# Optimization experiments

Hardware: AMD Instinct MI355X
Metric: run time of the kernel (lower is better)

The kernel has to match this reference:

```python
import jax, jax.numpy as jnp
import numpy as np

D_MODEL = 1024
NUM_HEADS = 16
HEAD_DIM = D_MODEL // NUM_HEADS
B, S = 2, 2048


def setup_inputs() -> dict:
    key = jax.random.key(0)
    ks = jax.random.split(key, 16)
    sd = 1.0 / np.sqrt(D_MODEL)
    def lin(k):
        kw, kb = jax.random.split(k)
        W = jax.random.uniform(kw, (D_MODEL, D_MODEL), jnp.float32, -sd, sd)
        b = jax.random.uniform(kb, (D_MODEL,), jnp.float32, -sd, sd)
        return W, b
    Wq, bq = lin(ks[0]); Wk, bk = lin(ks[1]); Wv, bv = lin(ks[2]); Wo, bo = lin(ks[3])
    return {
        'q': jax.random.normal(ks[4], (B, S, D_MODEL), jnp.float32),
        'k': jax.random.normal(ks[5], (B, S, D_MODEL), jnp.float32),
        'v': jax.random.normal(ks[6], (B, S, D_MODEL), jnp.float32),
        'phase': jax.random.normal(ks[7], (B,), jnp.float32),
        'Wq': Wq, 'bq': bq, 'Wk': Wk, 'bk': bk, 'Wv': Wv, 'bv': bv, 'Wo': Wo, 'bo': bo,
        'phase_coupling': jnp.zeros((1, NUM_HEADS, 1, 1), jnp.float32),
        'attention_scale': jnp.ones((1,), jnp.float32),
        'stability_factor': jnp.ones((1,), jnp.float32),
    }


def reference(q, k, v, phase, Wq, bq, Wk, bk, Wv, bv, Wo, bo,
              phase_coupling, attention_scale, stability_factor):
    batch, seq, _ = q.shape
    scale = HEAD_DIM ** -0.5

    def split_heads(x):  # [B,S,D] -> [B,H,S,hd]
        return x.reshape(batch, -1, NUM_HEADS, HEAD_DIM).transpose(0, 2, 1, 3)

    qh = split_heads(q @ Wq.T + bq)
    kh = split_heads(k @ Wk.T + bk)
    vh = split_heads(v @ Wv.T + bv)

    scores = jnp.einsum('bhqd,bhkd->bhqk', qh, kh) * (scale * attention_scale)
    # phase modulation: phase [B] -> [B,1,1,1]; scores *= 1 + coupling*sin(phase)
    phase_factor = jnp.sin(phase)[:, None, None, None]
    scores = scores * (1.0 + phase_coupling * phase_factor)

    attn_weights = jax.nn.softmax(scores, axis=-1)  # dropout is identity in eval
    out = jnp.einsum('bhqk,bhkd->bhqd', attn_weights, vh)
    out = out.transpose(0, 2, 1, 3).reshape(batch, seq, D_MODEL)
    out = (out @ Wo.T + bo) * stability_factor
    return out, attn_weights
```

## Files before the change

kernel.cpp:

```cpp
#include <hip/hip_runtime.h>
#include <hip/hip_bf16.h>
#include <cstdint>
#include <cstddef>

#define NH 16
#define HD 64
#define SS 2048
#define DM 1024
#define MTOT 4096

typedef __attribute__((ext_vector_type(8))) short short8;
typedef __attribute__((ext_vector_type(4))) float float4v;
typedef __attribute__((ext_vector_type(4))) int int4v;
typedef __attribute__((ext_vector_type(4))) unsigned short ushort4v;

__device__ __forceinline__ unsigned short f2bf(float f){
  unsigned int u = __builtin_bit_cast(unsigned int, f);
  u += 0x7FFFu + ((u >> 16) & 1u);
  return (unsigned short)(u >> 16);
}

__device__ __forceinline__ void gload16(const void* g, void* l){
  __builtin_amdgcn_global_load_lds((const __attribute__((address_space(1))) void*)g,
                                   (__attribute__((address_space(3))) void*)l, 16, 0, 0);
}

__global__ __launch_bounds__(256) void cvt_kernel(const float* __restrict__ src,
                                                  unsigned short* __restrict__ dst, int n){
  for (int i = (blockIdx.x*blockDim.x + threadIdx.x)*4; i < n; i += gridDim.x*blockDim.x*4){
    float4v v = *reinterpret_cast<const float4v*>(src + i);
    ushort4v o;
    o.x = f2bf(v.x); o.y = f2bf(v.y); o.z = f2bf(v.z); o.w = f2bf(v.w);
    *reinterpret_cast<ushort4v*>(dst + i) = o;
  }
}

template<int MODE>
__global__ __launch_bounds__(256) void gemm_bt(const unsigned short* __restrict__ A,
                                               const unsigned short* __restrict__ Bw,
                                               const float* __restrict__ bias,
                                               void* __restrict__ outp,
                                               int M, int N, int K,
                                               const float* __restrict__ oscale_p){
  __shared__ unsigned short Alds[128*32];
  __shared__ unsigned short Blds[128*32];
  const int t = threadIdx.x;
  const int l = t & 63;
  const int w = t >> 6;
  const int m0 = blockIdx.y * 128, n0 = blockIdx.x * 128;
  const int wm = (w & 1)*64, wn = (w >> 1)*64;
  const int srow = t >> 2;
  const int scol = (t & 3)*8;
  const int lr = l & 15, lg = l >> 4;
  float4v acc[4][4] = {};
  for (int k0 = 0; k0 < K; k0 += 32){
    __syncthreads();
    gload16(A  + (size_t)(m0 + srow     )*K + k0 + scol, Alds + t*8);
    gload16(A  + (size_t)(m0 + srow + 64)*K + k0 + scol, Alds + 2048 + t*8);
    gload16(Bw + (size_t)(n0 + srow     )*K + k0 + scol, Blds + t*8);
    gload16(Bw + (size_t)(n0 + srow + 64)*K + k0 + scol, Blds + 2048 + t*8);
    asm volatile("s_waitcnt vmcnt(0)" ::: "memory");
    __syncthreads();
    short8 afrag[4], bfrag[4];
    #pragma unroll
    for (int mb = 0; mb < 4; ++mb)
      afrag[mb] = *reinterpret_cast<const short8*>(Alds + (wm + mb*16 + lr)*32 + lg*8);
    #pragma unroll
    for (int nb = 0; nb < 4; ++nb)
      bfrag[nb] = *reinterpret_cast<const short8*>(Blds + (wn + nb*16 + lr)*32 + lg*8);
    #pragma unroll
    for (int mb = 0; mb < 4; ++mb)
      #pragma unroll
      for (int nb = 0; nb < 4; ++nb)
        acc[mb][nb] = __builtin_amdgcn_mfma_f32_16x16x32_bf16(afrag[mb], bfrag[nb], acc[mb][nb], 0, 0, 0);
  }
  const float osc = (MODE == 2) ? oscale_p[0] : 1.0f;
  #pragma unroll
  for (int mb = 0; mb < 4; ++mb){
    #pragma unroll
    for (int nb = 0; nb < 4; ++nb){
      const int gn = n0 + wn + nb*16 + lr;
      const float biasv = bias[gn];
      #pragma unroll
      for (int r = 0; r < 4; ++r){
        const int gm = m0 + wm + mb*16 + lg*4 + r;
        float v = acc[mb][nb][r] + biasv;
        if (MODE == 2){
          reinterpret_cast<float*>(outp)[(size_t)gm*N + gn] = v * osc;
        } else {
          const int b_ = gm >> 11, s_ = gm & 2047, h_ = gn >> 6, d_ = gn & 63;
          unsigned short* o = reinterpret_cast<unsigned short*>(outp);
          if (MODE == 0)
            o[((size_t)(b_*NH + h_)*SS + s_)*HD + d_] = f2bf(v);
          else
            o[((size_t)(b_*NH + h_)*HD + d_)*SS + s_] = f2bf(v);
        }
      }
    }
  }
}

__global__ __launch_bounds__(256, 4) void attn_kernel(
    const unsigned short* __restrict__ Qh,
    const unsigned short* __restrict__ Kh,
    const unsigned short* __restrict__ Vt,
    unsigned short* __restrict__ AO,
    float* __restrict__ attnW,
    const float* __restrict__ phase,
    const float* __restrict__ pc,
    const float* __restrict__ ascale)
{
  __shared__ float mred[4][32], lred[4][32];
  __shared__ __attribute__((aligned(16))) float ored[4][32*32];

  const int t = threadIdx.x;
  const int w = t >> 6, l = t & 63;
  const int lr = l & 15, lg = l >> 4;
  const int bh = blockIdx.x, qt = blockIdx.y;
  const int b = bh >> 4, h = bh & 15;
  const int q0 = qt*32;
  const float scale_eff = 0.125f * ascale[0] * (1.0f + pc[h] * sinf(phase[b]));

  const unsigned short* qbase = Qh + ((size_t)bh*SS + q0 + lr)*HD + lg*8;
  short8 aq[2][2];
  aq[0][0] = *reinterpret_cast<const short8*>(qbase);
  aq[0][1] = *reinterpret_cast<const short8*>(qbase + 32);
  aq[1][0] = *reinterpret_cast<const short8*>(qbase + 16*HD);
  aq[1][1] = *reinterpret_cast<const short8*>(qbase + 16*HD + 32);

  const int tbase = w * 512;
  const unsigned short* kbase = Kh + ((size_t)bh*SS + tbase + lr)*HD + lg*8;

  float m[2] = {-1e30f, -1e30f}, lsum[2] = {0.f, 0.f};
  #pragma unroll 2
  for (int tb = 0; tb < 32; ++tb){
    const unsigned short* kp = kbase + (size_t)tb*16*HD;
    short8 bk0 = *reinterpret_cast<const short8*>(kp);
    short8 bk1 = *reinterpret_cast<const short8*>(kp + 32);
    #pragma unroll
    for (int qs = 0; qs < 2; ++qs){
      float4v pacc = {};
      pacc = __builtin_amdgcn_mfma_f32_16x16x32_bf16(bk0, aq[qs][0], pacc, 0, 0, 0);
      pacc = __builtin_amdgcn_mfma_f32_16x16x32_bf16(bk1, aq[qs][1], pacc, 0, 0, 0);
      const float s0 = pacc[0]*scale_eff, s1 = pacc[1]*scale_eff;
      const float s2 = pacc[2]*scale_eff, s3 = pacc[3]*scale_eff;
      const float smax = fmaxf(fmaxf(s0, s1), fmaxf(s2, s3));
      const float nm = fmaxf(m[qs], smax);
      lsum[qs] = lsum[qs]*__expf(m[qs] - nm)
               + __expf(s0 - nm) + __expf(s1 - nm) + __expf(s2 - nm) + __expf(s3 - nm);
      m[qs] = nm;
    }
  }
  #pragma unroll
  for (int mask = 16; mask < 64; mask <<= 1){
    #pragma unroll
    for (int qs = 0; qs < 2; ++qs){
      float om = __shfl_xor(m[qs], mask, 64);
      float ol = __shfl_xor(lsum[qs], mask, 64);
      float nm = fmaxf(m[qs], om);
      lsum[qs] = lsum[qs]*__expf(m[qs] - nm) + ol*__expf(om - nm);
      m[qs] = nm;
    }
  }
  if (l < 16){
    mred[w][lr] = m[0];      lred[w][lr] = lsum[0];
    mred[w][16+lr] = m[1];   lred[w][16+lr] = lsum[1];
  }
  __syncthreads();
  float rm[2], rrl[2];
  #pragma unroll
  for (int qs = 0; qs < 2; ++qs){
    const int row = qs*16 + lr;
    float fm = mred[0][row], fl = lred[0][row];
    #pragma unroll
    for (int ww = 1; ww < 4; ++ww){
      float om = mred[ww][row], ol = lred[ww][row];
      float nm = fmaxf(fm, om);
      fl = fl*__expf(fm - nm) + ol*__expf(om - nm);
      fm = nm;
    }
    rm[qs] = fm; rrl[qs] = 1.0f/fl;
  }

  float4v oacc[2][4] = {};
  float* gwq0 = attnW + ((size_t)bh*SS + q0 + lr)*SS + tbase;
  float* gwq1 = gwq0 + (size_t)16*SS;
  const unsigned short* vbase = Vt + ((size_t)bh*HD + lr)*SS + tbase + lg*8;
  const int idxA = (((lg & 1)*2)*16 + lr)*4;
  const int idxB = idxA + 64;
  const bool hi = (lg >= 2);

  for (int tp = 0; tp < 16; ++tp){
    const int tloc = tp*32;
    const unsigned short* kpA = kbase + (size_t)tloc*HD;
    short8 k0A = *reinterpret_cast<const short8*>(kpA);
    short8 k1A = *reinterpret_cast<const short8*>(kpA + 32);
    short8 k0B = *reinterpret_cast<const short8*>(kpA + 16*HD);
    short8 k1B = *reinterpret_cast<const short8*>(kpA + 16*HD + 32);
    short8 bv[4];
    #pragma unroll
    for (int dt = 0; dt < 4; ++dt)
      bv[dt] = *reinterpret_cast<const short8*>(vbase + (size_t)(dt*16)*SS + tloc);

    #pragma unroll
    for (int qs = 0; qs < 2; ++qs){
      float4v pA = {};
      pA = __builtin_amdgcn_mfma_f32_16x16x32_bf16(k0A, aq[qs][0], pA, 0, 0, 0);
      pA = __builtin_amdgcn_mfma_f32_16x16x32_bf16(k1A, aq[qs][1], pA, 0, 0, 0);
      float4v pB = {};
      pB = __builtin_amdgcn_mfma_f32_16x16x32_bf16(k0B, aq[qs][0], pB, 0, 0, 0);
      pB = __builtin_amdgcn_mfma_f32_16x16x32_bf16(k1B, aq[qs][1], pB, 0, 0, 0);
      float4v eA, eB;
      eA.x = __expf(pA[0]*scale_eff - rm[qs])*rrl[qs];
      eA.y = __expf(pA[1]*scale_eff - rm[qs])*rrl[qs];
      eA.z = __expf(pA[2]*scale_eff - rm[qs])*rrl[qs];
      eA.w = __expf(pA[3]*scale_eff - rm[qs])*rrl[qs];
      eB.x = __expf(pB[0]*scale_eff - rm[qs])*rrl[qs];
      eB.y = __expf(pB[1]*scale_eff - rm[qs])*rrl[qs];
      eB.z = __expf(pB[2]*scale_eff - rm[qs])*rrl[qs];
      eB.w = __expf(pB[3]*scale_eff - rm[qs])*rrl[qs];
      const int w0A = ((int)f2bf(eA.y) << 16) | (int)f2bf(eA.x);
      const int w1A = ((int)f2bf(eA.w) << 16) | (int)f2bf(eA.z);
      const int w0B = ((int)f2bf(eB.y) << 16) | (int)f2bf(eB.x);
      const int w1B = ((int)f2bf(eB.w) << 16) | (int)f2bf(eB.z);

      const int a0 = __builtin_amdgcn_ds_bpermute(idxA, w0A);
      const int b0 = __builtin_amdgcn_ds_bpermute(idxA, w0B);
      const int a1 = __builtin_amdgcn_ds_bpermute(idxA, w1A);
      const int b1 = __builtin_amdgcn_ds_bpermute(idxA, w1B);
      const int a2 = __builtin_amdgcn_ds_bpermute(idxB, w0A);
      const int b2 = __builtin_amdgcn_ds_bpermute(idxB, w0B);
      const int a3 = __builtin_amdgcn_ds_bpermute(idxB, w1A);
      const int b3 = __builtin_amdgcn_ds_bpermute(idxB, w1B);
      int4v words;
      words.x = hi ? b0 : a0;
      words.y = hi ? b1 : a1;
      words.z = hi ? b2 : a2;
      words.w = hi ? b3 : a3;
      const short8 pa = __builtin_bit_cast(short8, words);

      #pragma unroll
      for (int dt = 0; dt < 4; ++dt)
        oacc[qs][dt] = __builtin_amdgcn_mfma_f32_16x16x32_bf16(pa, bv[dt], oacc[qs][dt], 0, 0, 0);

      float* gw = qs ? gwq1 : gwq0;
      __builtin_nontemporal_store(eA, reinterpret_cast<float4v*>(gw + tloc + lg*4));
      __builtin_nontemporal_store(eB, reinterpret_cast<float4v*>(gw + tloc + 16 + lg*4));
    }
  }

  #pragma unroll
  for (int c = 0; c < 2; ++c){
    if (c) __syncthreads();
    #pragma unroll
    for (int qs = 0; qs < 2; ++qs)
      #pragma unroll
      for (int dl = 0; dl < 2; ++dl)
        #pragma unroll
        for (int r = 0; r < 4; ++r)
          ored[w][(qs*16 + lg*4 + r)*32 + dl*16 + lr] = oacc[qs][c*2 + dl][r];
    __syncthreads();
    const int row = t >> 3, c4 = (t & 7);
    const float4v* o0 = reinterpret_cast<const float4v*>(&ored[0][0]);
    const int fi = row*8 + c4;
    float4v s = o0[fi];
    s += o0[fi + 256];
    s += o0[fi + 512];
    s += o0[fi + 768];
    ushort4v o4;
    o4.x = f2bf(s.x); o4.y = f2bf(s.y); o4.z = f2bf(s.z); o4.w = f2bf(s.w);
    *reinterpret_cast<ushort4v*>(AO + ((size_t)b*SS + q0 + row)*DM + h*HD + c*32 + c4*4) = o4;
  }
}

extern "C" void kernel_launch(void* const* d_in, const int* in_sizes, int n_in,
                              void* d_out, int out_size, void* d_ws, size_t ws_size,
                              hipStream_t stream){
  const float* q      = (const float*)d_in[0];
  const float* k      = (const float*)d_in[1];
  const float* v      = (const float*)d_in[2];
  const float* phase  = (const float*)d_in[3];
  const float* Wq     = (const float*)d_in[4];
  const float* bq     = (const float*)d_in[5];
  const float* Wk     = (const float*)d_in[6];
  const float* bk     = (const float*)d_in[7];
  const float* Wv     = (const float*)d_in[8];
  const float* bv     = (const float*)d_in[9];
  const float* Wo     = (const float*)d_in[10];
  const float* bo     = (const float*)d_in[11];
  const float* pc     = (const float*)d_in[12];
  const float* ascale = (const float*)d_in[13];
  const float* stab   = (const float*)d_in[14];

  unsigned short* Xq  = (unsigned short*)d_ws;
  unsigned short* Xk  = Xq  + 4194304;
  unsigned short* Xv  = Xk  + 4194304;
  unsigned short* Wqb = Xv  + 4194304;
  unsigned short* Wkb = Wqb + 1048576;
  unsigned short* Wvb = Wkb + 1048576;
  unsigned short* Wob = Wvb + 1048576;
  unsigned short* Qh  = Wob + 1048576;
  unsigned short* Kh  = Qh  + 4194304;
  unsigned short* Vt  = Kh  + 4194304;
  unsigned short* AO  = Vt  + 4194304;

  float* out0  = (float*)d_out;
  float* attnW = out0 + (size_t)MTOT*DM;

  cvt_kernel<<<512, 256, 0, stream>>>(q, Xq, MTOT*DM);
  cvt_kernel<<<512, 256, 0, stream>>>(k, Xk, MTOT*DM);
  cvt_kernel<<<512, 256, 0, stream>>>(v, Xv, MTOT*DM);
  cvt_kernel<<<256, 256, 0, stream>>>(Wq, Wqb, DM*DM);
  cvt_kernel<<<256, 256, 0, stream>>>(Wk, Wkb, DM*DM);
  cvt_kernel<<<256, 256, 0, stream>>>(Wv, Wvb, DM*DM);
  cvt_kernel<<<256, 256, 0, stream>>>(Wo, Wob, DM*DM);

  dim3 gg(DM/128, MTOT/128);
  gemm_bt<0><<<gg, 256, 0, stream>>>(Xq, Wqb, bq, Qh, MTOT, DM, DM, nullptr);
  gemm_bt<0><<<gg, 256, 0, stream>>>(Xk, Wkb, bk, Kh, MTOT, DM, DM, nullptr);
  gemm_bt<1><<<gg, 256, 0, stream>>>(Xv, Wvb, bv, Vt, MTOT, DM, DM, nullptr);

  attn_kernel<<<dim3(32, SS/32, 1), 256, 0, stream>>>(Qh, Kh, Vt, AO, attnW,
                                                      phase, pc, ascale);

  gemm_bt<2><<<gg, 256, 0, stream>>>(AO, Wob, bo, out0, MTOT, DM, DM, stab);
}
```

Baseline: 339.2 us.

## Batch conversion and QKV projection launches, use exp2 softmax, raise attention occupancy

```diff
diff --git a/kernel.cpp b/kernel.cpp
--- a/kernel.cpp
+++ b/kernel.cpp
@@ -2,6 +2,7 @@
 #include <hip/hip_bf16.h>
 #include <cstdint>
 #include <cstddef>
+#include <cmath>
 
 #define NH 16
 #define HD 64
@@ -25,8 +26,13 @@
                                    (__attribute__((address_space(3))) void*)l, 16, 0, 0);
 }
 
-__global__ __launch_bounds__(256) void cvt_kernel(const float* __restrict__ src,
-                                                  unsigned short* __restrict__ dst, int n){
+__global__ __launch_bounds__(256) void cvt3_kernel(
+    const float* __restrict__ s0, const float* __restrict__ s1, const float* __restrict__ s2,
+    unsigned short* __restrict__ d0, unsigned short* __restrict__ d1, unsigned short* __restrict__ d2,
+    int n){
+  const int z = blockIdx.z;
+  const float* src = z==0 ? s0 : (z==1 ? s1 : s2);
+  unsigned short* dst = z==0 ? d0 : (z==1 ? d1 : d2);
   for (int i = (blockIdx.x*blockDim.x + threadIdx.x)*4; i < n; i += gridDim.x*blockDim.x*4){
     float4v v = *reinterpret_cast<const float4v*>(src + i);
     ushort4v o;
@@ -35,15 +41,37 @@
   }
 }
 
-template<int MODE>
-__global__ __launch_bounds__(256) void gemm_bt(const unsigned short* __restrict__ A,
-                                               const unsigned short* __restrict__ Bw,
-                                               const float* __restrict__ bias,
-                                               void* __restrict__ outp,
-                                               int M, int N, int K,
-                                               const float* __restrict__ oscale_p){
+__global__ __launch_bounds__(256) void cvt4_kernel(
+    const float* __restrict__ s0, const float* __restrict__ s1,
+    const float* __restrict__ s2, const float* __restrict__ s3,
+    unsigned short* __restrict__ d0, unsigned short* __restrict__ d1,
+    unsigned short* __restrict__ d2, unsigned short* __restrict__ d3,
+    int n){
+  const int z = blockIdx.z;
+  const float* src = z==0 ? s0 : (z==1 ? s1 : (z==2 ? s2 : s3));
+  unsigned short* dst = z==0 ? d0 : (z==1 ? d1 : (z==2 ? d2 : d3));
+  for (int i = (blockIdx.x*blockDim.x + threadIdx.x)*4; i < n; i += gridDim.x*blockDim.x*4){
+    float4v v = *reinterpret_cast<const float4v*>(src + i);
+    ushort4v o;
+    o.x = f2bf(v.x); o.y = f2bf(v.y); o.z = f2bf(v.z); o.w = f2bf(v.w);
+    *reinterpret_cast<ushort4v*>(dst + i) = o;
+  }
+}
+
+__global__ __launch_bounds__(256) void gemm_proj(
+    const unsigned short* __restrict__ X0, const unsigned short* __restrict__ X1, const unsigned short* __restrict__ X2,
+    const unsigned short* __restrict__ W0, const unsigned short* __restrict__ W1, const unsigned short* __restrict__ W2,
+    const float* __restrict__ b0, const float* __restrict__ b1, const float* __restrict__ b2,
+    unsigned short* __restrict__ O0, unsigned short* __restrict__ O1, unsigned short* __restrict__ O2){
   __shared__ unsigned short Alds[128*32];
   __shared__ unsigned short Blds[128*32];
+  const int z = blockIdx.z;
+  const unsigned short* A  = z==0 ? X0 : (z==1 ? X1 : X2);
+  const unsigned short* Bw = z==0 ? W0 : (z==1 ? W1 : W2);
+  const float* bias        = z==0 ? b0 : (z==1 ? b1 : b2);
+  unsigned short* outp     = z==0 ? O0 : (z==1 ? O1 : O2);
+  const bool vmode = (z == 2);
+  const int K = DM, N = DM;
   const int t = threadIdx.x;
   const int l = t & 63;
   const int w = t >> 6;
@@ -74,7 +102,6 @@
       for (int nb = 0; nb < 4; ++nb)
         acc[mb][nb] = __builtin_amdgcn_mfma_f32_16x16x32_bf16(afrag[mb], bfrag[nb], acc[mb][nb], 0, 0, 0);
   }
-  const float osc = (MODE == 2) ? oscale_p[0] : 1.0f;
   #pragma unroll
   for (int mb = 0; mb < 4; ++mb){
     #pragma unroll
@@ -85,22 +112,71 @@
       for (int r = 0; r < 4; ++r){
         const int gm = m0 + wm + mb*16 + lg*4 + r;
         float v = acc[mb][nb][r] + biasv;
-        if (MODE == 2){
-          reinterpret_cast<float*>(outp)[(size_t)gm*N + gn] = v * osc;
-        } else {
-          const int b_ = gm >> 11, s_ = gm & 2047, h_ = gn >> 6, d_ = gn & 63;
-          unsigned short* o = reinterpret_cast<unsigned short*>(outp);
-          if (MODE == 0)
-            o[((size_t)(b_*NH + h_)*SS + s_)*HD + d_] = f2bf(v);
-          else
-            o[((size_t)(b_*NH + h_)*HD + d_)*SS + s_] = f2bf(v);
-        }
+        const int b_ = gm >> 11, s_ = gm & 2047, h_ = gn >> 6, d_ = gn & 63;
+        if (!vmode)
+          outp[((size_t)(b_*NH + h_)*SS + s_)*HD + d_] = f2bf(v);
+        else
+          outp[((size_t)(b_*NH + h_)*HD + d_)*SS + s_] = f2bf(v);
       }
     }
   }
 }
 
-__global__ __launch_bounds__(256, 4) void attn_kernel(
+__global__ __launch_bounds__(256) void gemm_out(const unsigned short* __restrict__ A,
+                                                const unsigned short* __restrict__ Bw,
+                                                const float* __restrict__ bias,
+                                                float* __restrict__ outp,
+                                                const float* __restrict__ oscale_p){
+  __shared__ unsigned short Alds[128*32];
+  __shared__ unsigned short Blds[128*32];
+  const int K = DM, N = DM;
+  const int t = threadIdx.x;
+  const int l = t & 63;
+  const int w = t >> 6;
+  const int m0 = blockIdx.y * 128, n0 = blockIdx.x * 128;
+  const int wm = (w & 1)*64, wn = (w >> 1)*64;
+  const int srow = t >> 2;
+  const int scol = (t & 3)*8;
+  const int lr = l & 15, lg = l >> 4;
+  float4v acc[4][4] = {};
+  for (int k0 = 0; k0 < K; k0 += 32){
+    __syncthreads();
+    gload16(A  + (size_t)(m0 + srow     )*K + k0 + scol, Alds + t*8);
+    gload16(A  + (size_t)(m0 + srow + 64)*K + k0 + scol, Alds + 2048 + t*8);
+    gload16(Bw + (size_t)(n0 + srow     )*K + k0 + scol, Blds + t*8);
+    gload16(Bw + (size_t)(n0 + srow + 64)*K + k0 + scol, Blds + 2048 + t*8);
+    asm volatile("s_waitcnt vmcnt(0)" ::: "memory");
+    __syncthreads();
+    short8 afrag[4], bfrag[4];
+    #pragma unroll
+    for (int mb = 0; mb < 4; ++mb)
+      afrag[mb] = *reinterpret_cast<const short8*>(Alds + (wm + mb*16 + lr)*32 + lg*8);
+    #pragma unroll
+    for (int nb = 0; nb < 4; ++nb)
+      bfrag[nb] = *reinterpret_cast<const short8*>(Blds + (wn + nb*16 + lr)*32 + lg*8);
+    #pragma unroll
+    for (int mb = 0; mb < 4; ++mb)
+      #pragma unroll
+      for (int nb = 0; nb < 4; ++nb)
+        acc[mb][nb] = __builtin_amdgcn_mfma_f32_16x16x32_bf16(afrag[mb], bfrag[nb], acc[mb][nb], 0, 0, 0);
+  }
+  const float osc = oscale_p[0];
+  #pragma unroll
+  for (int mb = 0; mb < 4; ++mb){
+    #pragma unroll
+    for (int nb = 0; nb < 4; ++nb){
+      const int gn = n0 + wn + nb*16 + lr;
+      const float biasv = bias[gn];
+      #pragma unroll
+      for (int r = 0; r < 4; ++r){
+        const int gm = m0 + wm + mb*16 + lg*4 + r;
+        outp[(size_t)gm*N + gn] = (acc[mb][nb][r] + biasv) * osc;
+      }
+    }
+  }
+}
+
+__global__ __launch_bounds__(256, 6) void attn_kernel(
     const unsigned short* __restrict__ Qh,
     const unsigned short* __restrict__ Kh,
     const unsigned short* __restrict__ Vt,
@@ -119,7 +195,8 @@
   const int bh = blockIdx.x, qt = blockIdx.y;
   const int b = bh >> 4, h = bh & 15;
   const int q0 = qt*32;
-  const float scale_eff = 0.125f * ascale[0] * (1.0f + pc[h] * sinf(phase[b]));
+  const float scale2 = 0.125f * ascale[0] * (1.0f + pc[h] * sinf(phase[b]))
+                       * 1.4426950408889634f;
 
   const unsigned short* qbase = Qh + ((size_t)bh*SS + q0 + lr)*HD + lg*8;
   short8 aq[2][2];
@@ -142,12 +219,12 @@
       float4v pacc = {};
       pacc = __builtin_amdgcn_mfma_f32_16x16x32_bf16(bk0, aq[qs][0], pacc, 0, 0, 0);
       pacc = __builtin_amdgcn_mfma_f32_16x16x32_bf16(bk1, aq[qs][1], pacc, 0, 0, 0);
-      const float s0 = pacc[0]*scale_eff, s1 = pacc[1]*scale_eff;
-      const float s2 = pacc[2]*scale_eff, s3 = pacc[3]*scale_eff;
+      const float s0 = pacc[0]*scale2, s1 = pacc[1]*scale2;
+      const float s2 = pacc[2]*scale2, s3 = pacc[3]*scale2;
       const float smax = fmaxf(fmaxf(s0, s1), fmaxf(s2, s3));
       const float nm = fmaxf(m[qs], smax);
-      lsum[qs] = lsum[qs]*__expf(m[qs] - nm)
-               + __expf(s0 - nm) + __expf(s1 - nm) + __expf(s2 - nm) + __expf(s3 - nm);
+      lsum[qs] = lsum[qs]*exp2f(m[qs] - nm)
+               + exp2f(s0 - nm) + exp2f(s1 - nm) + exp2f(s2 - nm) + exp2f(s3 - nm);
       m[qs] = nm;
     }
   }
@@ -158,7 +235,7 @@
       float om = __shfl_xor(m[qs], mask, 64);
       float ol = __shfl_xor(lsum[qs], mask, 64);
       float nm = fmaxf(m[qs], om);
-      lsum[qs] = lsum[qs]*__expf(m[qs] - nm) + ol*__expf(om - nm);
+      lsum[qs] = lsum[qs]*exp2f(m[qs] - nm) + ol*exp2f(om - nm);
       m[qs] = nm;
     }
   }
@@ -176,7 +253,7 @@
     for (int ww = 1; ww < 4; ++ww){
       float om = mred[ww][row], ol = lred[ww][row];
       float nm = fmaxf(fm, om);
-      fl = fl*__expf(fm - nm) + ol*__expf(om - nm);
+      fl = fl*exp2f(fm - nm) + ol*exp2f(om - nm);
       fm = nm;
     }
     rm[qs] = fm; rrl[qs] = 1.0f/fl;
@@ -211,14 +288,14 @@
       pB = __builtin_amdgcn_mfma_f32_16x16x32_bf16(k0B, aq[qs][0], pB, 0, 0, 0);
       pB = __builtin_amdgcn_mfma_f32_16x16x32_bf16(k1B, aq[qs][1], pB, 0, 0, 0);
       float4v eA, eB;
-      eA.x = __expf(pA[0]*scale_eff - rm[qs])*rrl[qs];
-      eA.y = __expf(pA[1]*scale_eff - rm[qs])*rrl[qs];
-      eA.z = __expf(pA[2]*scale_eff - rm[qs])*rrl[qs];
-      eA.w = __expf(pA[3]*scale_eff - rm[qs])*rrl[qs];
-      eB.x = __expf(pB[0]*scale_eff - rm[qs])*rrl[qs];
-      eB.y = __expf(pB[1]*scale_eff - rm[qs])*rrl[qs];
-      eB.z = __expf(pB[2]*scale_eff - rm[qs])*rrl[qs];
-      eB.w = __expf(pB[3]*scale_eff - rm[qs])*rrl[qs];
+      eA.x = exp2f(pA[0]*scale2 - rm[qs])*rrl[qs];
+      eA.y = exp2f(pA[1]*scale2 - rm[qs])*rrl[qs];
+      eA.z = exp2f(pA[2]*scale2 - rm[qs])*rrl[qs];
+      eA.w = exp2f(pA[3]*scale2 - rm[qs])*rrl[qs];
+      eB.x = exp2f(pB[0]*scale2 - rm[qs])*rrl[qs];
+      eB.y = exp2f(pB[1]*scale2 - rm[qs])*rrl[qs];
+      eB.z = exp2f(pB[2]*scale2 - rm[qs])*rrl[qs];
+      eB.w = exp2f(pB[3]*scale2 - rm[qs])*rrl[qs];
       const int w0A = ((int)f2bf(eA.y) << 16) | (int)f2bf(eA.x);
       const int w1A = ((int)f2bf(eA.w) << 16) | (int)f2bf(eA.z);
       const int w0B = ((int)f2bf(eB.y) << 16) | (int)f2bf(eB.x);
@@ -307,21 +384,14 @@
   float* out0  = (float*)d_out;
   float* attnW = out0 + (size_t)MTOT*DM;
 
-  cvt_kernel<<<512, 256, 0, stream>>>(q, Xq, MTOT*DM);
-  cvt_kernel<<<512, 256, 0, stream>>>(k, Xk, MTOT*DM);
-  cvt_kernel<<<512, 256, 0, stream>>>(v, Xv, MTOT*DM);
-  cvt_kernel<<<256, 256, 0, stream>>>(Wq, Wqb, DM*DM);
-  cvt_kernel<<<256, 256, 0, stream>>>(Wk, Wkb, DM*DM);
-  cvt_kernel<<<256, 256, 0, stream>>>(Wv, Wvb, DM*DM);
-  cvt_kernel<<<256, 256, 0, stream>>>(Wo, Wob, DM*DM);
-
-  dim3 gg(DM/128, MTOT/128);
-  gemm_bt<0><<<gg, 256, 0, stream>>>(Xq, Wqb, bq, Qh, MTOT, DM, DM, nullptr);
-  gemm_bt<0><<<gg, 256, 0, stream>>>(Xk, Wkb, bk, Kh, MTOT, DM, DM, nullptr);
-  gemm_bt<1><<<gg, 256, 0, stream>>>(Xv, Wvb, bv, Vt, MTOT, DM, DM, nullptr);
+  cvt3_kernel<<<dim3(512,1,3), 256, 0, stream>>>(q, k, v, Xq, Xk, Xv, MTOT*DM);
+  cvt4_kernel<<<dim3(128,1,4), 256, 0, stream>>>(Wq, Wk, Wv, Wo, Wqb, Wkb, Wvb, Wob, DM*DM);
+
+  gemm_proj<<<dim3(DM/128, MTOT/128, 3), 256, 0, stream>>>(
+      Xq, Xk, Xv, Wqb, Wkb, Wvb, bq, bk, bv, Qh, Kh, Vt);
 
   attn_kernel<<<dim3(32, SS/32, 1), 256, 0, stream>>>(Qh, Kh, Vt, AO, attnW,
                                                       phase, pc, ascale);
 
-  gemm_bt<2><<<gg, 256, 0, stream>>>(AO, Wob, bo, out0, MTOT, DM, DM, stab);
-}
+  gemm_out<<<dim3(DM/128, MTOT/128, 1), 256, 0, stream>>>(AO, Wob, bo, out0, stab);
+}
```

Result: slower. 464.8 us (+37.0%).
